# Kernel tuning notes

Hardware: AMD Instinct MI355X
Metric: run time of the kernel (lower is better)

The kernel has to match this reference:

```python
import jax, jax.numpy as jnp
import numpy as np

NEG = -1e10

def setup_inputs() -> dict:
    key = jax.random.key(0)
    ks = jax.random.split(key, 12)
    B, W, V, D, R, VOCAB = 16, 64, 64, 256, 64, 50000
    head_ctx = jax.random.randint(ks[0], (B, W), 0, VOCAB)
    tail_ctx = jax.random.randint(ks[1], (B, V), 0, VOCAB)
    emb = jax.random.normal(ks[2], (VOCAB, D), dtype=jnp.float32) * 0.02
    rela_mat = jax.random.normal(ks[3], (R, D), dtype=jnp.float32) * 0.02
    fc_w = jax.random.normal(ks[4], (3 * D, D), dtype=jnp.float32) * (1.0 / np.sqrt(3 * D))
    fc_b = jnp.zeros((D,), jnp.float32)
    att_w1 = jax.random.normal(ks[5], (D, D), dtype=jnp.float32) * (1.0 / np.sqrt(D))
    att_b1 = jnp.zeros((D,), jnp.float32)
    att_w2 = jax.random.normal(ks[6], (D, 1), dtype=jnp.float32) * (1.0 / np.sqrt(D))
    att_b2 = jnp.zeros((1,), jnp.float32)
    out_w = jax.random.normal(ks[7], (D, 1), dtype=jnp.float32) * (1.0 / np.sqrt(D))
    out_b = jnp.zeros((1,), jnp.float32)
    return {"head_ctx": head_ctx, "tail_ctx": tail_ctx, "emb": emb, "rela_mat": rela_mat,
            "fc_w": fc_w, "fc_b": fc_b, "att_w1": att_w1, "att_b1": att_b1,
            "att_w2": att_w2, "att_b2": att_b2, "out_w": out_w, "out_b": out_b}

def reference(head_ctx, tail_ctx, emb, rela_mat, fc_w, fc_b, att_w1, att_b1, att_w2, att_b2, out_w, out_b):
    A = emb[head_ctx]            # [B, W, D]
    Bt = emb[tail_ctx]           # [B, V, D]
    Bsz, W, D = A.shape
    V = Bt.shape[1]
    R = rela_mat.shape[0]
    N = W * V
    # DistMult scoring for every (head_i, tail_j, rela_r) triple, no repeat materialization
    scores = jnp.einsum('bid,bjd,rd->bijr', A, Bt, rela_mat).reshape(Bsz, N, R)
    # cut_rela_score: mask relations not beating the null (last) relation
    null = scores[:, :, -1:]
    scores = jnp.where(scores <= null, NEG, scores)
    norm_scores = jax.nn.softmax(scores, axis=-1)            # [B, N, R]
    rela_vec = jnp.einsum('bnr,rd->bnd', norm_scores, rela_mat)
    # tuple (i,j) pairing: index n = i*V + j
    A_rep = jnp.broadcast_to(A[:, :, None, :], (Bsz, W, V, D)).reshape(Bsz, N, D)
    B_rep = jnp.broadcast_to(Bt[:, None, :, :], (Bsz, W, V, D)).reshape(Bsz, N, D)
    tuple_vec = jnp.tanh(jnp.concatenate([A_rep, B_rep, rela_vec], axis=-1) @ fc_w + fc_b)  # [B, N, D]
    # tuple attention pooling
    att = jnp.tanh(tuple_vec @ att_w1 + att_b1) @ att_w2 + att_b2   # [B, N, 1]
    att_norms = jax.nn.softmax(att, axis=1)                          # [B, N, 1]
    fuse = jnp.sum(att_norms * tuple_vec, axis=1)                    # [B, D]
    logits = (fuse @ out_w + out_b).squeeze(-1)                      # [B]
    return logits, att_norms, norm_scores
```

## Files before the change

### kernel.cpp

```cpp
#include <hip/hip_runtime.h>
#include <hip/hip_bf16.h>

#define NB 16
#define NW 64
#define NV 64
#define ND 256
#define NR 64
#define NN 4096
#define NEGV -10000000000.0f

typedef __attribute__((ext_vector_type(8))) short short8;
typedef __attribute__((ext_vector_type(4))) float f32x4;

__device__ inline float cvt(const void* p, int idx, int flag) {
  if (flag) return __bfloat162float(((const __hip_bfloat16*)p)[idx]);
  return ((const float*)p)[idx];
}
__device__ inline void stv(void* p, int idx, float v, int flag) {
  if (flag) ((__hip_bfloat16*)p)[idx] = __float2bfloat16(v);
  else ((float*)p)[idx] = v;
}
__device__ inline float bf2f(short s) {
  return __uint_as_float(((unsigned int)(unsigned short)s) << 16);
}
__device__ inline float tanh_fast(float x) {
  float ax = fabsf(x);
  float e = __expf(-2.f * ax);
  float r = (1.f - e) / (1.f + e);
  return copysignf(r, x);
}

__global__ void k_detect(const unsigned int* embw, int* flagp) {
  __shared__ float red[256];
  int t = threadIdx.x;
  float mx = 0.f;
  for (int i = t; i < 1024; i += 256) {
    unsigned int w = embw[i];
    unsigned int fb = (w & 0xffffu) << 16;
    float a = fabsf(__uint_as_float(fb));
    if (!(a < 1e9f)) a = 1e9f;
    mx = fmaxf(mx, a);
  }
  red[t] = mx;
  __syncthreads();
  for (int s = 128; s > 0; s >>= 1) {
    if (t < s) red[t] = fmaxf(red[t], red[t + s]);
    __syncthreads();
  }
  if (t == 0) flagp[0] = (red[0] < 1000.f) ? 1 : 0;
}

__global__ void k_prep(const void* rela, float* relaT,
                       const void* b1, const void* w2, const void* outw,
                       const void* b2, const void* outb, float* sp,
                       const void* w1, __hip_bfloat16* w1b,
                       const int* head, const int* tail, const void* emb,
                       float* Af, float* Bf, const int* flagp) {
  int flag = flagp[0];
  int blk = blockIdx.x;
  int t = threadIdx.x;
  if (blk < 64) {
    relaT[t * NR + blk] = cvt(rela, blk * ND + t, flag);
  } else if (blk == 64) {
    sp[t] = cvt(b1, t, flag);
    sp[256 + t] = cvt(w2, t, flag);
    sp[512 + t] = cvt(outw, t, flag);
    if (t == 0) {
      sp[768] = cvt(b2, 0, flag);
      sp[769] = cvt(outb, 0, flag);
    }
  } else if (blk < 321) {
    int flat = (blk - 65) * 256 + t;
    int i = flat & 7;
    int lane = (flat >> 3) & 63;
    int kst = (flat >> 9) & 7;
    int nt = flat >> 12;
    int k = kst * 32 + (lane >> 4) * 8 + i;
    int n = nt * 16 + (lane & 15);
    w1b[flat] = __float2bfloat16(cvt(w1, k * ND + n, flag));
  } else {
    int row = blk - 321;
    if (row < NB * NW) {
      int ix = head[row];
      Af[row * ND + t] = cvt(emb, ix * ND + t, flag);
    } else {
      int rr = row - NB * NW;
      int ix = tail[rr];
      Bf[rr * ND + t] = cvt(emb, ix * ND + t, flag);
    }
  }
}

__global__ void __launch_bounds__(256) k_premm(const float* __restrict__ Af,
                                               const float* __restrict__ Bf,
                                               const void* __restrict__ rela,
                                               const void* __restrict__ fcw,
                                               const void* __restrict__ fcb,
                                               float* __restrict__ Ah,
                                               float* __restrict__ Bh,
                                               __hip_bfloat16* __restrict__ rwb,
                                               const int* __restrict__ flagp) {
  int flag = flagp[0];
  int blk = blockIdx.x;
  int t = threadIdx.x;
  __shared__ float rl[4][ND];
  int base, wbase, addb = 0, isr = 0;
  const float* src = Af;
  if (blk < 256) { base = blk * 4; wbase = 0; addb = 1; }
  else if (blk < 512) { base = (blk - 256) * 4; src = Bf; wbase = ND; }
  else { base = (blk - 512) * 4; wbase = 2 * ND; isr = 1; }
#pragma unroll
  for (int i = 0; i < 4; ++i)
    rl[i][t] = isr ? cvt(rela, (base + i) * ND + t, flag)
                   : src[(base + i) * ND + t];
  __syncthreads();
  float acc0 = 0.f, acc1 = 0.f, acc2 = 0.f, acc3 = 0.f;
  const f32x4* r0p = (const f32x4*)rl[0];
  const f32x4* r1p = (const f32x4*)rl[1];
  const f32x4* r2p = (const f32x4*)rl[2];
  const f32x4* r3p = (const f32x4*)rl[3];
#pragma unroll 4
  for (int k4 = 0; k4 < 64; ++k4) {
    float w0 = cvt(fcw, (wbase + k4 * 4 + 0) * ND + t, flag);
    float w1v = cvt(fcw, (wbase + k4 * 4 + 1) * ND + t, flag);
    float w2v = cvt(fcw, (wbase + k4 * 4 + 2) * ND + t, flag);
    float w3v = cvt(fcw, (wbase + k4 * 4 + 3) * ND + t, flag);
    f32x4 r0 = r0p[k4], r1 = r1p[k4], r2 = r2p[k4], r3 = r3p[k4];
    acc0 += r0.x * w0 + r0.y * w1v + r0.z * w2v + r0.w * w3v;
    acc1 += r1.x * w0 + r1.y * w1v + r1.z * w2v + r1.w * w3v;
    acc2 += r2.x * w0 + r2.y * w1v + r2.z * w2v + r2.w * w3v;
    acc3 += r3.x * w0 + r3.y * w1v + r3.z * w2v + r3.w * w3v;
  }
  float bias = addb ? cvt(fcb, t, flag) : 0.f;
  float res[4] = {acc0 + bias, acc1 + bias, acc2 + bias, acc3 + bias};
  if (!isr) {
    float* dst = addb ? Ah : Bh;
#pragma unroll
    for (int i = 0; i < 4; ++i) dst[(base + i) * ND + t] = res[i];
  } else {
#pragma unroll
    for (int i = 0; i < 4; ++i) {
      int rr = base + i;
      int ks = rr >> 5, ii = rr & 7, lh = (rr >> 3) & 3;
      int nt = t >> 4, ll = t & 15;
      int flat = ((nt * 2 + ks) * 64 + lh * 16 + ll) * 8 + ii;
      rwb[flat] = __float2bfloat16(res[i]);
    }
  }
}

__global__ void __launch_bounds__(256) k_scores(const float* __restrict__ Af,
                                                const float* __restrict__ Bf,
                                                const float* __restrict__ relaT,
                                                void* __restrict__ out,
                                                __hip_bfloat16* __restrict__ nsb,
                                                const int* __restrict__ flagp) {
  int flag = flagp[0];
  int bi = blockIdx.x;
  int b = bi >> 6;
  int t = threadIdx.x;
  int r = t & 63;
  int q = __builtin_amdgcn_readfirstlane(t >> 6);
  __shared__ float Al[ND];
  __shared__ float part[2][4 * 256];
  Al[t] = Af[bi * ND + t];
  __syncthreads();
  float preR[64];
#pragma unroll
  for (int i2 = 0; i2 < 64; ++i2) {
    int d = q * 64 + i2;
    preR[i2] = Al[d] * relaT[d * NR + r];
  }
  const float* __restrict__ Bbase = Bf + (size_t)b * NV * ND + q * 64;
  for (int jg = 0; jg < 16; ++jg) {
    float* pb = part[jg & 1];
#pragma unroll
    for (int jj = 0; jj < 4; ++jj) {
      const float* __restrict__ Bj = Bbase + (size_t)(jg * 4 + jj) * ND;
      float acc = 0.f;
#pragma unroll
      for (int i4 = 0; i4 < 16; ++i4) {
        acc += preR[i4 * 4 + 0] * Bj[i4 * 4 + 0];
        acc += preR[i4 * 4 + 1] * Bj[i4 * 4 + 1];
        acc += preR[i4 * 4 + 2] * Bj[i4 * 4 + 2];
        acc += preR[i4 * 4 + 3] * Bj[i4 * 4 + 3];
      }
      pb[jj * 256 + t] = acc;
    }
    __syncthreads();
    {
      int j4 = q;
      float s = pb[j4 * 256 + r] + pb[j4 * 256 + 64 + r]
              + pb[j4 * 256 + 128 + r] + pb[j4 * 256 + 192 + r];
      float nullv = __shfl(s, 63, 64);
      float m = (s <= nullv) ? NEGV : s;
      float mx = m;
#pragma unroll
      for (int o = 32; o > 0; o >>= 1) mx = fmaxf(mx, __shfl_xor(mx, o, 64));
      float e = __expf(m - mx);
      float sum = e;
#pragma unroll
      for (int o = 32; o > 0; o >>= 1) sum += __shfl_xor(sum, o, 64);
      float ns = e / sum;
      int j = jg * 4 + j4;
      int nidx = (bi * 64 + j) * 64 + r;
      stv(out, 16 + NB * NN + nidx, ns, flag);
      nsb[nidx] = __float2bfloat16(ns);
    }
  }
}

__global__ void __launch_bounds__(256) k_tuple2(const __hip_bfloat16* __restrict__ nsb,
                                                const __hip_bfloat16* __restrict__ rwb,
                                                const float* __restrict__ Ah,
                                                const float* __restrict__ Bh,
                                                __hip_bfloat16* __restrict__ tup) {
  int t = threadIdx.x;
  int wv = t >> 6, lane = t & 63;
  int bi = blockIdx.x;
  int b = bi >> 6;
  const short* nsS = (const short*)nsb;
  const short* rwS = (const short*)rwb;
  int m = lane & 15;
  int kgrp = lane >> 4;
  f32x4 acc[16];
#pragma unroll
  for (int i = 0; i < 16; ++i) acc[i] = (f32x4){0.f, 0.f, 0.f, 0.f};
  int nrow = bi * 64 + wv * 16 + m;
#pragma unroll
  for (int ks = 0; ks < 2; ++ks) {
    short8 a = *(const short8*)(nsS + (size_t)nrow * 64 + ks * 32 + kgrp * 8);
#pragma unroll
    for (int nt = 0; nt < 16; ++nt) {
      short8 bfr = *(const short8*)(rwS + (((nt * 2 + ks) * 64 + lane) << 3));
      acc[nt] = __builtin_amdgcn_mfma_f32_16x16x32_bf16(a, bfr, acc[nt], 0, 0, 0);
    }
  }
  int rbase = bi * 64 + wv * 16 + (lane >> 4) * 4;
  int jbase = rbase & 63;
#pragma unroll
  for (int nt = 0; nt < 16; ++nt) {
    int col = nt * 16 + m;
    float ahv = Ah[bi * ND + col];
#pragma unroll
    for (int reg = 0; reg < 4; ++reg) {
      int ng = rbase + reg;
      float v = acc[nt][reg] + ahv + Bh[(size_t)(b * 64 + jbase + reg) * ND + col];
      tup[(size_t)ng * ND + col] = __float2bfloat16(tanh_fast(v));
    }
  }
}

__global__ void __launch_bounds__(256) k_att2(const __hip_bfloat16* __restrict__ tup,
                                              const __hip_bfloat16* __restrict__ w1b,
                                              const float* __restrict__ sp,
                                              float* __restrict__ att_raw,
                                              float* __restrict__ dotv) {
  int t = threadIdx.x;
  int wv = t >> 6, lane = t & 63;
  int r0 = blockIdx.x * 128 + wv * 32;
  const short* tupS = (const short*)tup;
  const short* w1S = (const short*)w1b;
  const float* owf = sp + 512;
  float b2v = sp[768];

  f32x4 acc0[16], acc1[16];
#pragma unroll
  for (int i = 0; i < 16; ++i) {
    acc0[i] = (f32x4){0.f, 0.f, 0.f, 0.f};
    acc1[i] = (f32x4){0.f, 0.f, 0.f, 0.f};
  }
  float dp0 = 0.f, dp1 = 0.f;
  int arow0 = r0 + (lane & 15);
  int arow1 = arow0 + 16;
  int kgrp = lane >> 4;

#pragma unroll
  for (int ks = 0; ks < 8; ++ks) {
    int k0 = ks * 32 + kgrp * 8;
    short8 a0 = *(const short8*)(tupS + (size_t)arow0 * ND + k0);
    short8 a1 = *(const short8*)(tupS + (size_t)arow1 * ND + k0);
#pragma unroll
    for (int i = 0; i < 8; ++i) {
      float w = owf[k0 + i];
      dp0 += bf2f(a0[i]) * w;
      dp1 += bf2f(a1[i]) * w;
    }
#pragma unroll
    for (int nt = 0; nt < 16; ++nt) {
      short8 bfr = *(const short8*)(w1S + (((nt * 8 + ks) * 64 + lane) << 3));
      acc0[nt] = __builtin_amdgcn_mfma_f32_16x16x32_bf16(a0, bfr, acc0[nt], 0, 0, 0);
      acc1[nt] = __builtin_amdgcn_mfma_f32_16x16x32_bf16(a1, bfr, acc1[nt], 0, 0, 0);
    }
  }

  dp0 += __shfl_xor(dp0, 16, 64); dp0 += __shfl_xor(dp0, 32, 64);
  dp1 += __shfl_xor(dp1, 16, 64); dp1 += __shfl_xor(dp1, 32, 64);
  if (lane < 16) {
    dotv[r0 + lane] = dp0;
    dotv[r0 + 16 + lane] = dp1;
  }

  float p0[4] = {0.f, 0.f, 0.f, 0.f};
  float p1[4] = {0.f, 0.f, 0.f, 0.f};
#pragma unroll
  for (int nt = 0; nt < 16; ++nt) {
    int col = nt * 16 + (lane & 15);
    float b1v = sp[col];
    float w2v = sp[256 + col];
#pragma unroll
    for (int reg = 0; reg < 4; ++reg) {
      p0[reg] += tanh_fast(acc0[nt][reg] + b1v) * w2v;
      p1[reg] += tanh_fast(acc1[nt][reg] + b1v) * w2v;
    }
  }
#pragma unroll
  for (int o = 1; o < 16; o <<= 1) {
#pragma unroll
    for (int reg = 0; reg < 4; ++reg) {
      p0[reg] += __shfl_xor(p0[reg], o, 64);
      p1[reg] += __shfl_xor(p1[reg], o, 64);
    }
  }
  if ((lane & 15) == 0) {
    int rb = r0 + (lane >> 4) * 4;
#pragma unroll
    for (int reg = 0; reg < 4; ++reg) {
      att_raw[rb + reg] = p0[reg] + b2v;
      att_raw[rb + 16 + reg] = p1[reg] + b2v;
    }
  }
}

__global__ void k_fuse(const float* att_raw, const float* dotv,
                       const float* sp, void* out, const int* flagp) {
  int flag = flagp[0];
  int b = blockIdx.x;
  int t = threadIdx.x;
  __shared__ float red[256];
  float vals[16];
  float mx = -3.4e38f;
#pragma unroll
  for (int c = 0; c < 16; ++c) {
    vals[c] = att_raw[b * NN + c * 256 + t];
    mx = fmaxf(mx, vals[c]);
  }
  red[t] = mx;
  __syncthreads();
  for (int s = 128; s > 0; s >>= 1) {
    if (t < s) red[t] = fmaxf(red[t], red[t + s]);
    __syncthreads();
  }
  float M = red[0];
  __syncthreads();
  float sm = 0.f;
#pragma unroll
  for (int c = 0; c < 16; ++c) {
    vals[c] = __expf(vals[c] - M);
    sm += vals[c];
  }
  red[t] = sm;
  __syncthreads();
  for (int s = 128; s > 0; s >>= 1) {
    if (t < s) red[t] += red[t + s];
    __syncthreads();
  }
  float Z = red[0];
  __syncthreads();
  float acc = 0.f;
#pragma unroll
  for (int c = 0; c < 16; ++c) {
    int n = c * 256 + t;
    float a = vals[c] / Z;
    stv(out, 16 + b * NN + n, a, flag);
    acc += a * dotv[b * NN + n];
  }
  red[t] = acc;
  __syncthreads();
  for (int s = 128; s > 0; s >>= 1) {
    if (t < s) red[t] += red[t + s];
    __syncthreads();
  }
  if (t == 0) stv(out, b, red[0] + sp[769], flag);
}

extern "C" void kernel_launch(void* const* d_in, const int* in_sizes, int n_in,
                              void* d_out, int out_size, void* d_ws, size_t ws_size,
                              hipStream_t stream) {
  const int* head = (const int*)d_in[0];
  const int* tail = (const int*)d_in[1];
  const void* emb = d_in[2];
  const void* rela = d_in[3];
  const void* fcw = d_in[4];
  const void* fcb = d_in[5];
  const void* w1 = d_in[6];
  const void* b1 = d_in[7];
  const void* w2 = d_in[8];
  const void* b2 = d_in[9];
  const void* outw = d_in[10];
  const void* outb = d_in[11];

  float* ws = (float*)d_ws;
  int* flagp = (int*)d_ws;
  const size_t O_RELAT = 16;
  const size_t O_AF = O_RELAT + 16384;
  const size_t O_BF = O_AF + 262144;
  const size_t O_AH = O_BF + 262144;
  const size_t O_BH = O_AH + 262144;
  const size_t O_ATTR = O_BH + 262144;
  const size_t O_DOT = O_ATTR + 65536;
  const size_t O_SP = O_DOT + 65536;
  const size_t O_W1B = O_SP + 1024;
  const size_t O_RWB = O_W1B + 32768;
  const size_t O_NSB = O_RWB + 8192;
  const size_t O_TUP = O_NSB + 2097152;

  float* relaT = ws + O_RELAT;
  float* Af = ws + O_AF;
  float* Bf = ws + O_BF;
  float* Ah = ws + O_AH;
  float* Bh = ws + O_BH;
  float* attr = ws + O_ATTR;
  float* dotv = ws + O_DOT;
  float* sp = ws + O_SP;
  __hip_bfloat16* w1b = (__hip_bfloat16*)(ws + O_W1B);
  __hip_bfloat16* rwb = (__hip_bfloat16*)(ws + O_RWB);
  __hip_bfloat16* nsb = (__hip_bfloat16*)(ws + O_NSB);
  __hip_bfloat16* tup = (__hip_bfloat16*)(ws + O_TUP);

  hipLaunchKernelGGL(k_detect, dim3(1), dim3(256), 0, stream,
                     (const unsigned int*)emb, flagp);
  hipLaunchKernelGGL(k_prep, dim3(2369), dim3(256), 0, stream,
                     rela, relaT, b1, w2, outw, b2, outb, sp,
                     w1, w1b, head, tail, emb, Af, Bf, flagp);
  hipLaunchKernelGGL(k_premm, dim3(528), dim3(256), 0, stream,
                     Af, Bf, rela, fcw, fcb, Ah, Bh, rwb, flagp);
  hipLaunchKernelGGL(k_scores, dim3(1024), dim3(256), 0, stream,
                     Af, Bf, relaT, d_out, nsb, flagp);
  hipLaunchKernelGGL(k_tuple2, dim3(1024), dim3(256), 0, stream,
                     nsb, rwb, Ah, Bh, tup);
  hipLaunchKernelGGL(k_att2, dim3(512), dim3(256), 0, stream,
                     tup, w1b, sp, attr, dotv);
  hipLaunchKernelGGL(k_fuse, dim3(16), dim3(256), 0, stream,
                     attr, dotv, sp, d_out, flagp);
}
```

Before: 262.5 us.

## Stage B rows through LDS with software pipelining in scores; halve att2 rows per wave

```diff
diff --git a/kernel.cpp b/kernel.cpp
--- a/kernel.cpp
+++ b/kernel.cpp
@@ -160,10 +160,12 @@
   int b = bi >> 6;
   int t = threadIdx.x;
   int r = t & 63;
-  int q = __builtin_amdgcn_readfirstlane(t >> 6);
+  int q = t >> 6;
   __shared__ float Al[ND];
+  __shared__ float Bl[2][4 * ND];
   __shared__ float part[2][4 * 256];
   Al[t] = Af[bi * ND + t];
+  f32x4 pre = *(const f32x4*)(Bf + ((size_t)b * NV + q) * ND + r * 4);
   __syncthreads();
   float preR[64];
 #pragma unroll
@@ -171,27 +173,18 @@
     int d = q * 64 + i2;
     preR[i2] = Al[d] * relaT[d * NR + r];
   }
-  const float* __restrict__ Bbase = Bf + (size_t)b * NV * ND + q * 64;
+
   for (int jg = 0; jg < 16; ++jg) {
-    float* pb = part[jg & 1];
-#pragma unroll
-    for (int jj = 0; jj < 4; ++jj) {
-      const float* __restrict__ Bj = Bbase + (size_t)(jg * 4 + jj) * ND;
-      float acc = 0.f;
-#pragma unroll
-      for (int i4 = 0; i4 < 16; ++i4) {
-        acc += preR[i4 * 4 + 0] * Bj[i4 * 4 + 0];
-        acc += preR[i4 * 4 + 1] * Bj[i4 * 4 + 1];
-        acc += preR[i4 * 4 + 2] * Bj[i4 * 4 + 2];
-        acc += preR[i4 * 4 + 3] * Bj[i4 * 4 + 3];
-      }
-      pb[jj * 256 + t] = acc;
-    }
+    int buf = jg & 1;
+    *(f32x4*)(&Bl[buf][q * ND + r * 4]) = pre;
+    if (jg < 15)
+      pre = *(const f32x4*)(Bf + ((size_t)b * NV + (jg + 1) * 4 + q) * ND + r * 4);
     __syncthreads();
-    {
-      int j4 = q;
-      float s = pb[j4 * 256 + r] + pb[j4 * 256 + 64 + r]
-              + pb[j4 * 256 + 128 + r] + pb[j4 * 256 + 192 + r];
+
+    if (jg > 0) {
+      const float* pb = part[1 - buf];
+      float s = pb[q * 256 + r] + pb[q * 256 + 64 + r]
+              + pb[q * 256 + 128 + r] + pb[q * 256 + 192 + r];
       float nullv = __shfl(s, 63, 64);
       float m = (s <= nullv) ? NEGV : s;
       float mx = m;
@@ -202,11 +195,47 @@
 #pragma unroll
       for (int o = 32; o > 0; o >>= 1) sum += __shfl_xor(sum, o, 64);
       float ns = e / sum;
-      int j = jg * 4 + j4;
+      int j = (jg - 1) * 4 + q;
       int nidx = (bi * 64 + j) * 64 + r;
       stv(out, 16 + NB * NN + nidx, ns, flag);
       nsb[nidx] = __float2bfloat16(ns);
     }
+
+    const f32x4* Bl4 = (const f32x4*)Bl[buf];
+#pragma unroll
+    for (int jj = 0; jj < 4; ++jj) {
+      float acc = 0.f;
+      int ib = jj * 64 + q * 16;
+#pragma unroll
+      for (int i4 = 0; i4 < 16; ++i4) {
+        f32x4 bv = Bl4[ib + i4];
+        acc += preR[i4 * 4 + 0] * bv.x;
+        acc += preR[i4 * 4 + 1] * bv.y;
+        acc += preR[i4 * 4 + 2] * bv.z;
+        acc += preR[i4 * 4 + 3] * bv.w;
+      }
+      part[buf][jj * 256 + t] = acc;
+    }
+  }
+  __syncthreads();
+  {
+    const float* pb = part[1];
+    float s = pb[q * 256 + r] + pb[q * 256 + 64 + r]
+            + pb[q * 256 + 128 + r] + pb[q * 256 + 192 + r];
+    float nullv = __shfl(s, 63, 64);
+    float m = (s <= nullv) ? NEGV : s;
+    float mx = m;
+#pragma unroll
+    for (int o = 32; o > 0; o >>= 1) mx = fmaxf(mx, __shfl_xor(mx, o, 64));
+    float e = __expf(m - mx);
+    float sum = e;
+#pragma unroll
+    for (int o = 32; o > 0; o >>= 1) sum += __shfl_xor(sum, o, 64);
+    float ns = e / sum;
+    int j = 15 * 4 + q;
+    int nidx = (bi * 64 + j) * 64 + r;
+    stv(out, 16 + NB * NN + nidx, ns, flag);
+    nsb[nidx] = __float2bfloat16(ns);
   }
 }
 
@@ -258,77 +287,58 @@
                                               float* __restrict__ dotv) {
   int t = threadIdx.x;
   int wv = t >> 6, lane = t & 63;
-  int r0 = blockIdx.x * 128 + wv * 32;
+  int r0 = blockIdx.x * 64 + wv * 16;
   const short* tupS = (const short*)tup;
   const short* w1S = (const short*)w1b;
   const float* owf = sp + 512;
   float b2v = sp[768];
 
-  f32x4 acc0[16], acc1[16];
-#pragma unroll
-  for (int i = 0; i < 16; ++i) {
-    acc0[i] = (f32x4){0.f, 0.f, 0.f, 0.f};
-    acc1[i] = (f32x4){0.f, 0.f, 0.f, 0.f};
-  }
-  float dp0 = 0.f, dp1 = 0.f;
-  int arow0 = r0 + (lane & 15);
-  int arow1 = arow0 + 16;
+  f32x4 acc[16];
+#pragma unroll
+  for (int i = 0; i < 16; ++i) acc[i] = (f32x4){0.f, 0.f, 0.f, 0.f};
+  float dp = 0.f;
+  int arow = r0 + (lane & 15);
   int kgrp = lane >> 4;
 
 #pragma unroll
   for (int ks = 0; ks < 8; ++ks) {
     int k0 = ks * 32 + kgrp * 8;
-    short8 a0 = *(const short8*)(tupS + (size_t)arow0 * ND + k0);
-    short8 a1 = *(const short8*)(tupS + (size_t)arow1 * ND + k0);
-#pragma unroll
-    for (int i = 0; i < 8; ++i) {
-      float w = owf[k0 + i];
-      dp0 += bf2f(a0[i]) * w;
-      dp1 += bf2f(a1[i]) * w;
-    }
+    short8 a = *(const short8*)(tupS + (size_t)arow * ND + k0);
+#pragma unroll
+    for (int i = 0; i < 8; ++i)
+      dp += bf2f(a[i]) * owf[k0 + i];
 #pragma unroll
     for (int nt = 0; nt < 16; ++nt) {
       short8 bfr = *(const short8*)(w1S + (((nt * 8 + ks) * 64 + lane) << 3));
-      acc0[nt] = __builtin_amdgcn_mfma_f32_16x16x32_bf16(a0, bfr, acc0[nt], 0, 0, 0);
-      acc1[nt] = __builtin_amdgcn_mfma_f32_16x16x32_bf16(a1, bfr, acc1[nt], 0, 0, 0);
-    }
-  }
-
-  dp0 += __shfl_xor(dp0, 16, 64); dp0 += __shfl_xor(dp0, 32, 64);
-  dp1 += __shfl_xor(dp1, 16, 64); dp1 += __shfl_xor(dp1, 32, 64);
-  if (lane < 16) {
-    dotv[r0 + lane] = dp0;
-    dotv[r0 + 16 + lane] = dp1;
-  }
+      acc[nt] = __builtin_amdgcn_mfma_f32_16x16x32_bf16(a, bfr, acc[nt], 0, 0, 0);
+    }
+  }
+
+  dp += __shfl_xor(dp, 16, 64);
+  dp += __shfl_xor(dp, 32, 64);
+  if (lane < 16) dotv[r0 + lane] = dp;
 
   float p0[4] = {0.f, 0.f, 0.f, 0.f};
-  float p1[4] = {0.f, 0.f, 0.f, 0.f};
 #pragma unroll
   for (int nt = 0; nt < 16; ++nt) {
     int col = nt * 16 + (lane & 15);
     float b1v = sp[col];
     float w2v = sp[256 + col];
 #pragma unroll
-    for (int reg = 0; reg < 4; ++reg) {
-      p0[reg] += tanh_fast(acc0[nt][reg] + b1v) * w2v;
-      p1[reg] += tanh_fast(acc1[nt][reg] + b1v) * w2v;
-    }
+    for (int reg = 0; reg < 4; ++reg)
+      p0[reg] += tanh_fast(acc[nt][reg] + b1v) * w2v;
   }
 #pragma unroll
   for (int o = 1; o < 16; o <<= 1) {
 #pragma unroll
-    for (int reg = 0; reg < 4; ++reg) {
+    for (int reg = 0; reg < 4; ++reg)
       p0[reg] += __shfl_xor(p0[reg], o, 64);
-      p1[reg] += __shfl_xor(p1[reg], o, 64);
-    }
   }
   if ((lane & 15) == 0) {
     int rb = r0 + (lane >> 4) * 4;
 #pragma unroll
-    for (int reg = 0; reg < 4; ++reg) {
+    for (int reg = 0; reg < 4; ++reg)
       att_raw[rb + reg] = p0[reg] + b2v;
-      att_raw[rb + 16 + reg] = p1[reg] + b2v;
-    }
   }
 }
 
@@ -439,7 +449,7 @@
                      Af, Bf, relaT, d_out, nsb, flagp);
   hipLaunchKernelGGL(k_tuple2, dim3(1024), dim3(256), 0, stream,
                      nsb, rwb, Ah, Bh, tup);
-  hipLaunchKernelGGL(k_att2, dim3(512), dim3(256), 0, stream,
+  hipLaunchKernelGGL(k_att2, dim3(1024), dim3(256), 0, stream,
                      tup, w1b, sp, attr, dotv);
   hipLaunchKernelGGL(k_fuse, dim3(16), dim3(256), 0, stream,
                      attr, dotv, sp, d_out, flagp);
```

Measured after the change: 259.3 us. About the same (-1.2%).
